# Kernel optimization log

Hardware: AMD Instinct MI355X
Metric: run time of the kernel (lower is better)

Reference implementation:

```python
import jax, jax.numpy as jnp
import numpy as np

N_NODES = 100_000
N_EDGES = 1_000_000
NODE_DIM = 64
EDGE_DIM = 32
EPS = 1e-5
SLOPE = 0.1  # LeakyReLU negative slope


def _mlp2(v, W1, b1, W2, b2):
    # Linear -> LeakyReLU(0.1) -> (dropout = identity in eval) -> Linear
    h = jax.nn.leaky_relu(v @ W1 + b1, negative_slope=SLOPE)
    return h @ W2 + b2


def setup_inputs() -> dict:
    key = jax.random.key(0)
    ks = jax.random.split(key, 8)
    s = 0.05  # small init scale for weights
    return {
        "x": jax.random.normal(ks[0], (N_NODES, NODE_DIM), dtype=jnp.float32),
        "edge_attr": jax.random.normal(ks[1], (N_EDGES, EDGE_DIM), dtype=jnp.float32),
        # node_transform: Linear(D, 2D) -> Linear(2D, D)
        "W1n": jax.random.normal(ks[2], (NODE_DIM, 2 * NODE_DIM), dtype=jnp.float32) * s,
        "b1n": jnp.zeros((2 * NODE_DIM,), dtype=jnp.float32),
        "W2n": jax.random.normal(ks[3], (2 * NODE_DIM, NODE_DIM), dtype=jnp.float32) * s,
        "b2n": jnp.zeros((NODE_DIM,), dtype=jnp.float32),
        # edge_feature_transform: Linear(ED, D) -> Linear(D, D)
        "W1e": jax.random.normal(ks[4], (EDGE_DIM, NODE_DIM), dtype=jnp.float32) * s,
        "b1e": jnp.zeros((NODE_DIM,), dtype=jnp.float32),
        "W2e": jax.random.normal(ks[5], (NODE_DIM, NODE_DIM), dtype=jnp.float32) * s,
        "b2e": jnp.zeros((NODE_DIM,), dtype=jnp.float32),
        "res_w": jnp.ones((1,), dtype=jnp.float32),
        "dp_scale": jnp.ones((1,), dtype=jnp.float32),
        "gamma": jnp.ones((NODE_DIM,), dtype=jnp.float32),
        "beta": jnp.zeros((NODE_DIM,), dtype=jnp.float32),
        "edge_index": jax.random.randint(ks[6], (2, N_EDGES), 0, N_NODES, dtype=jnp.int64)
        if jax.config.jax_enable_x64 else jax.random.randint(ks[6], (2, N_EDGES), 0, N_NODES, dtype=jnp.int32),
    }


def reference(x, edge_attr, W1n, b1n, W2n, b2n, W1e, b1e, W2e, b2e,
              res_w, dp_scale, gamma, beta, edge_index):
    num_nodes = x.shape[0]
    # node_transform MLP on all nodes
    x_t = _mlp2(x, W1n, b1n, W2n, b2n)                 # [N, D]
    # edge_feature_transform MLP on all edges
    e_t = _mlp2(edge_attr, W1e, b1e, W2e, b2e)         # [E, D]
    src, dst = edge_index[0], edge_index[1]
    # per-edge gather-mul-scale, scatter-add into dst nodes
    msgs = x_t[src] * e_t * dp_scale                   # [E, D]
    aggregated = jax.ops.segment_sum(msgs, dst, num_segments=num_nodes)  # [N, D]
    out = x + aggregated * res_w
    # LayerNorm over last dim (dropout is identity in eval)
    mu = jnp.mean(out, axis=-1, keepdims=True)
    var = jnp.mean(jnp.square(out - mu), axis=-1, keepdims=True)
    return (out - mu) * jax.lax.rsqrt(var + EPS) * gamma + beta
```

## Files before the change

### kernel.cpp

```cpp
#include <hip/hip_runtime.h>
#include <hip/hip_bf16.h>

#define N_NODES 100000
#define N_EDGES 1000000
#define EPS 1e-5f
#define SLOPE 0.1f

typedef __attribute__((ext_vector_type(8))) short short8;
typedef __attribute__((ext_vector_type(4))) float f32x4;

#define MFMA16(a, b, c) __builtin_amdgcn_mfma_f32_16x16x32_bf16(a, b, c, 0, 0, 0)

__device__ __forceinline__ float lrelu(float v) { return v > 0.f ? v : SLOPE * v; }

__device__ __forceinline__ unsigned short f2bf(float f) {
  __hip_bfloat16 h = __float2bfloat16(f);
  return __builtin_bit_cast(unsigned short, h);
}
__device__ __forceinline__ unsigned pk2(float lo, float hi) {
  return (unsigned)f2bf(lo) | ((unsigned)f2bf(hi) << 16);
}
__device__ __forceinline__ float blo(unsigned u) { return __uint_as_float(u << 16); }
__device__ __forceinline__ float bhi(unsigned u) { return __uint_as_float(u & 0xffff0000u); }

__device__ __forceinline__ short8 mk_frag8(const float v[8]) {
  uint4 u;
  u.x = pk2(v[0], v[1]);
  u.y = pk2(v[2], v[3]);
  u.z = pk2(v[4], v[5]);
  u.w = pk2(v[6], v[7]);
  return __builtin_bit_cast(short8, u);
}

#if __has_builtin(__builtin_amdgcn_global_atomic_fadd_v2bf16)
#define AGG_BF16 1
typedef __attribute__((ext_vector_type(2))) short bf16x2;
typedef __attribute__((address_space(1))) bf16x2 gbf16x2;
__device__ __forceinline__ void atomic_pk_bf16(void* p, unsigned packed) {
  __builtin_amdgcn_global_atomic_fadd_v2bf16((gbf16x2*)(unsigned long long)p,
                                             __builtin_bit_cast(bf16x2, packed));
}
#else
#define AGG_BF16 0
#endif

__global__ __launch_bounds__(256) void node_mfma(const float* __restrict__ x,
                                                 const float* __restrict__ W1n,
                                                 const float* __restrict__ b1n,
                                                 const float* __restrict__ W2n,
                                                 const float* __restrict__ b2n,
                                                 __hip_bfloat16* __restrict__ xt) {
  const int lane = threadIdx.x & 63;
  const int lo = lane & 15;
  const int G = lane >> 4;
  const int wid = (blockIdx.x * blockDim.x + threadIdx.x) >> 6;
  const int nw = (gridDim.x * blockDim.x) >> 6;

  short8 A1[8][2];
#pragma unroll
  for (int t = 0; t < 8; ++t)
#pragma unroll
    for (int kt = 0; kt < 2; ++kt) {
      float v[8];
#pragma unroll
      for (int j = 0; j < 8; ++j) v[j] = W1n[(kt * 32 + G * 8 + j) * 128 + t * 16 + lo];
      A1[t][kt] = mk_frag8(v);
    }
  short8 A2[4][4];
#pragma unroll
  for (int ct = 0; ct < 4; ++ct)
#pragma unroll
    for (int kt = 0; kt < 4; ++kt) {
      float v[8];
#pragma unroll
      for (int j = 0; j < 8; ++j) v[j] = W2n[(kt * 32 + G * 8 + j) * 64 + ct * 16 + lo];
      A2[ct][kt] = mk_frag8(v);
    }
  const f32x4 zero = {0.f, 0.f, 0.f, 0.f};

  for (int tile = wid; tile < N_NODES / 16; tile += nw) {
    const int n0 = tile * 16;
    short8 B1[2];
#pragma unroll
    for (int kt = 0; kt < 2; ++kt) {
      const float* p = &x[(size_t)(n0 + lo) * 64 + kt * 32 + G * 8];
      float4 q0 = *(const float4*)p;
      float4 q1 = *(const float4*)(p + 4);
      float v[8] = {q0.x, q0.y, q0.z, q0.w, q1.x, q1.y, q1.z, q1.w};
      B1[kt] = mk_frag8(v);
    }
    unsigned P[8][2];
#pragma unroll
    for (int t = 0; t < 8; ++t) {
      f32x4 d = MFMA16(A1[t][0], B1[0], zero);
      d = MFMA16(A1[t][1], B1[1], d);
      const float4 bv = *(const float4*)&b1n[t * 16 + G * 4];
      P[t][0] = pk2(lrelu(d[0] + bv.x), lrelu(d[1] + bv.y));
      P[t][1] = pk2(lrelu(d[2] + bv.z), lrelu(d[3] + bv.w));
    }
    f32x4 D2[4] = {zero, zero, zero, zero};
#pragma unroll
    for (int kt = 0; kt < 4; ++kt) {
      unsigned u[4];
#pragma unroll
      for (int i = 0; i < 4; ++i) {
        const int srcidx = lo + 16 * (2 * (G & 1) + (i >> 1));
        unsigned r0 = (unsigned)__shfl((int)P[kt * 2][i & 1], srcidx);
        unsigned r1 = (unsigned)__shfl((int)P[kt * 2 + 1][i & 1], srcidx);
        u[i] = (lane >= 32) ? r1 : r0;
      }
      uint4 uu;
      uu.x = u[0]; uu.y = u[1]; uu.z = u[2]; uu.w = u[3];
      short8 B2 = __builtin_bit_cast(short8, uu);
#pragma unroll
      for (int ct = 0; ct < 4; ++ct) D2[ct] = MFMA16(A2[ct][kt], B2, D2[ct]);
    }
    unsigned short* row = (unsigned short*)xt + (size_t)(n0 + lo) * 64;
#pragma unroll
    for (int ct = 0; ct < 4; ++ct) {
      const float4 bv = *(const float4*)&b2n[ct * 16 + G * 4];
      uint2 s;
      s.x = pk2(D2[ct][0] + bv.x, D2[ct][1] + bv.y);
      s.y = pk2(D2[ct][2] + bv.z, D2[ct][3] + bv.w);
      *(uint2*)(row + ct * 16 + G * 4) = s;
    }
  }
}

__global__ __launch_bounds__(256) void edge_mfma(const float* __restrict__ ea,
                                                 const int* __restrict__ ei,
                                                 const float* __restrict__ W1e,
                                                 const float* __restrict__ b1e,
                                                 const float* __restrict__ W2e,
                                                 const float* __restrict__ b2e,
                                                 const __hip_bfloat16* __restrict__ xt,
                                                 const float* __restrict__ dp,
                                                 void* __restrict__ aggv) {
  const int lane = threadIdx.x & 63;
  const int lo = lane & 15;
  const int G = lane >> 4;
  const int w = threadIdx.x >> 6;
  const int wid = (blockIdx.x * blockDim.x + threadIdx.x) >> 6;
  const int nw = (gridDim.x * blockDim.x) >> 6;
  const float scale = dp[0];

  __shared__ float msg_lds[4][16 * 68];
  float* ml = &msg_lds[w][0];

  short8 A1[4];
#pragma unroll
  for (int t = 0; t < 4; ++t) {
    float v[8];
#pragma unroll
    for (int j = 0; j < 8; ++j) v[j] = W1e[(G * 8 + j) * 64 + t * 16 + lo];
    A1[t] = mk_frag8(v);
  }
  short8 A2[4][2];
#pragma unroll
  for (int t = 0; t < 4; ++t)
#pragma unroll
    for (int kt = 0; kt < 2; ++kt) {
      float v[8];
#pragma unroll
      for (int j = 0; j < 8; ++j) v[j] = W2e[(kt * 32 + G * 8 + j) * 64 + t * 16 + lo];
      A2[t][kt] = mk_frag8(v);
    }
  f32x4 Cb1[4], Cb2[4];
#pragma unroll
  for (int t = 0; t < 4; ++t)
#pragma unroll
    for (int r = 0; r < 4; ++r) {
      Cb1[t][r] = b1e[t * 16 + G * 4 + r];
      Cb2[t][r] = b2e[t * 16 + G * 4 + r];
    }

  for (int tile = wid; tile < N_EDGES / 16; tile += nw) {
    const int e0 = tile * 16;
    const int srcv = ei[e0 + lo];
    const int dstv = ei[N_EDGES + e0 + lo];
    const float* p = &ea[(size_t)(e0 + lo) * 32 + G * 8];
    float4 q0 = *(const float4*)p;
    float4 q1 = *(const float4*)(p + 4);
    float v[8] = {q0.x, q0.y, q0.z, q0.w, q1.x, q1.y, q1.z, q1.w};
    short8 B1 = mk_frag8(v);

    unsigned P[4][2];
#pragma unroll
    for (int t = 0; t < 4; ++t) {
      f32x4 d = MFMA16(A1[t], B1, Cb1[t]);
      P[t][0] = pk2(lrelu(d[0]), lrelu(d[1]));
      P[t][1] = pk2(lrelu(d[2]), lrelu(d[3]));
    }
    short8 B2f[2];
#pragma unroll
    for (int kt = 0; kt < 2; ++kt) {
      unsigned u[4];
#pragma unroll
      for (int i = 0; i < 4; ++i) {
        const int srcidx = lo + 16 * (2 * (G & 1) + (i >> 1));
        unsigned r0 = (unsigned)__shfl((int)P[kt * 2][i & 1], srcidx);
        unsigned r1 = (unsigned)__shfl((int)P[kt * 2 + 1][i & 1], srcidx);
        u[i] = (lane >= 32) ? r1 : r0;
      }
      uint4 uu;
      uu.x = u[0]; uu.y = u[1]; uu.z = u[2]; uu.w = u[3];
      B2f[kt] = __builtin_bit_cast(short8, uu);
    }
#pragma unroll
    for (int t = 0; t < 4; ++t) {
      f32x4 d = MFMA16(A2[t][0], B2f[0], Cb2[t]);
      d = MFMA16(A2[t][1], B2f[1], d);
      f32x4 sv;
#pragma unroll
      for (int r = 0; r < 4; ++r) sv[r] = d[r] * scale;
      *(f32x4*)&ml[lo * 68 + t * 16 + G * 4] = sv;
    }

#if AGG_BF16
    const int half = lane >> 5;
    const int l2 = lane & 31;
    unsigned short* aggb = (unsigned short*)aggv;
#pragma unroll
    for (int ep = 0; ep < 8; ++ep) {
      const int e = 2 * ep + half;
      const int se = __shfl(srcv, e);
      const int de = __shfl(dstv, e);
      const float2 m = *(const float2*)&ml[e * 68 + 2 * l2];
      const unsigned g = *(const unsigned*)((const unsigned short*)xt + (size_t)se * 64 + 2 * l2);
      atomic_pk_bf16(aggb + (size_t)de * 64 + 2 * l2, pk2(blo(g) * m.x, bhi(g) * m.y));
    }
#else
    float* agg = (float*)aggv;
#pragma unroll
    for (int eb = 0; eb < 2; ++eb) {
      float msg[8];
      int des[8];
#pragma unroll
      for (int i = 0; i < 8; ++i) {
        const int e = eb * 8 + i;
        const int se = __builtin_amdgcn_readlane(srcv, e);
        des[i] = __builtin_amdgcn_readlane(dstv, e);
        const float m = ml[e * 68 + lane];
        const unsigned short xb = ((const unsigned short*)xt)[(size_t)se * 64 + lane];
        msg[i] = __uint_as_float((unsigned)xb << 16) * m;
      }
#pragma unroll
      for (int i = 0; i < 8; ++i)
        unsafeAtomicAdd(agg + (size_t)des[i] * 64 + lane, msg[i]);
    }
#endif
  }
}

__global__ __launch_bounds__(256) void finalize(const float* __restrict__ x,
                                                const void* __restrict__ aggv,
                                                const float* __restrict__ res_w,
                                                const float* __restrict__ gamma,
                                                const float* __restrict__ beta,
                                                float* __restrict__ out) {
  const int lane = threadIdx.x & 63;
  const int wid = (blockIdx.x * blockDim.x + threadIdx.x) >> 6;
  const int nw = (gridDim.x * blockDim.x) >> 6;
  const float rw = res_w[0];
  const float g = gamma[lane], bb = beta[lane];
  for (int n = wid; n < N_NODES; n += nw) {
#if AGG_BF16
    const unsigned short ab = ((const unsigned short*)aggv)[(size_t)n * 64 + lane];
    const float a = __uint_as_float((unsigned)ab << 16);
#else
    const float a = ((const float*)aggv)[(size_t)n * 64 + lane];
#endif
    float v = fmaf(a, rw, x[(size_t)n * 64 + lane]);
    float s = v;
#pragma unroll
    for (int off = 1; off < 64; off <<= 1) s += __shfl_xor(s, off);
    const float mu = s * (1.f / 64.f);
    const float d = v - mu;
    float s2 = d * d;
#pragma unroll
    for (int off = 1; off < 64; off <<= 1) s2 += __shfl_xor(s2, off);
    out[(size_t)n * 64 + lane] = fmaf(d * rsqrtf(s2 * (1.f / 64.f) + EPS), g, bb);
  }
}

extern "C" void kernel_launch(void* const* d_in, const int* in_sizes, int n_in,
                              void* d_out, int out_size, void* d_ws, size_t ws_size,
                              hipStream_t stream) {
  const float* x = (const float*)d_in[0];
  const float* edge_attr = (const float*)d_in[1];
  const float* W1n = (const float*)d_in[2];
  const float* b1n = (const float*)d_in[3];
  const float* W2n = (const float*)d_in[4];
  const float* b2n = (const float*)d_in[5];
  const float* W1e = (const float*)d_in[6];
  const float* b1e = (const float*)d_in[7];
  const float* W2e = (const float*)d_in[8];
  const float* b2e = (const float*)d_in[9];
  const float* res_w = (const float*)d_in[10];
  const float* dp_scale = (const float*)d_in[11];
  const float* gamma = (const float*)d_in[12];
  const float* beta = (const float*)d_in[13];
  const int* edge_index = (const int*)d_in[14];
  float* out = (float*)d_out;

  __hip_bfloat16* xt = (__hip_bfloat16*)d_ws;
  void* agg = (void*)((char*)d_ws + (size_t)N_NODES * 64 * sizeof(__hip_bfloat16));
#if AGG_BF16
  const size_t agg_bytes = (size_t)N_NODES * 64 * sizeof(__hip_bfloat16);
#else
  const size_t agg_bytes = (size_t)N_NODES * 64 * sizeof(float);
#endif

  hipMemsetAsync(agg, 0, agg_bytes, stream);
  node_mfma<<<1024, 256, 0, stream>>>(x, W1n, b1n, W2n, b2n, xt);
  edge_mfma<<<2048, 256, 0, stream>>>(edge_attr, edge_index, W1e, b1e, W2e, b2e,
                                      xt, dp_scale, agg);
  finalize<<<1024, 256, 0, stream>>>(x, agg, res_w, gamma, beta, out);
}
```

Before: 166.0 us.

## Fold aggregate zeroing into node kernel and prefetch edge gathers early

The separate memset of the aggregation buffer is removed, and the node kernel now zeroes it with a grid-stride loop, which saves one launch. In the edge kernel, the src/dst indices and the bf16 x_t gathers for each lane's edges are loaded at the start of each tile, so their memory latency overlaps the two MFMA layers. This replaces the later shuffles of srcv/dstv. The trade-off is higher register pressure from holding 8 indices and 8 gathered words per lane, which could lower occupancy.

```diff
diff --git a/kernel.cpp b/kernel.cpp
--- a/kernel.cpp
+++ b/kernel.cpp
@@ -49,12 +49,19 @@
                                                  const float* __restrict__ b1n,
                                                  const float* __restrict__ W2n,
                                                  const float* __restrict__ b2n,
-                                                 __hip_bfloat16* __restrict__ xt) {
+                                                 __hip_bfloat16* __restrict__ xt,
+                                                 uint4* __restrict__ agg_zero,
+                                                 int agg_zero_n) {
   const int lane = threadIdx.x & 63;
   const int lo = lane & 15;
   const int G = lane >> 4;
-  const int wid = (blockIdx.x * blockDim.x + threadIdx.x) >> 6;
-  const int nw = (gridDim.x * blockDim.x) >> 6;
+  const int tid = blockIdx.x * blockDim.x + threadIdx.x;
+  const int nt = gridDim.x * blockDim.x;
+  const int wid = tid >> 6;
+  const int nw = nt >> 6;
+
+  const uint4 z = {0u, 0u, 0u, 0u};
+  for (int i = tid; i < agg_zero_n; i += nt) agg_zero[i] = z;
 
   short8 A1[8][2];
 #pragma unroll
@@ -174,10 +181,31 @@
       Cb2[t][r] = b2e[t * 16 + G * 4 + r];
     }
 
+#if AGG_BF16
+  const int half = lane >> 5;
+  const int l2 = lane & 31;
+  unsigned short* aggb = (unsigned short*)aggv;
+#endif
+
   for (int tile = wid; tile < N_EDGES / 16; tile += nw) {
     const int e0 = tile * 16;
+
+#if AGG_BF16
+    int se_r[8], de_r[8];
+#pragma unroll
+    for (int ep = 0; ep < 8; ++ep) {
+      se_r[ep] = ei[e0 + 2 * ep + half];
+      de_r[ep] = ei[N_EDGES + e0 + 2 * ep + half];
+    }
+    unsigned g_r[8];
+#pragma unroll
+    for (int ep = 0; ep < 8; ++ep)
+      g_r[ep] = *(const unsigned*)((const unsigned short*)xt + (size_t)se_r[ep] * 64 + 2 * l2);
+#else
     const int srcv = ei[e0 + lo];
     const int dstv = ei[N_EDGES + e0 + lo];
+#endif
+
     const float* p = &ea[(size_t)(e0 + lo) * 32 + G * 8];
     float4 q0 = *(const float4*)p;
     float4 q1 = *(const float4*)(p + 4);
@@ -217,17 +245,12 @@
     }
 
 #if AGG_BF16
-    const int half = lane >> 5;
-    const int l2 = lane & 31;
-    unsigned short* aggb = (unsigned short*)aggv;
 #pragma unroll
     for (int ep = 0; ep < 8; ++ep) {
       const int e = 2 * ep + half;
-      const int se = __shfl(srcv, e);
-      const int de = __shfl(dstv, e);
       const float2 m = *(const float2*)&ml[e * 68 + 2 * l2];
-      const unsigned g = *(const unsigned*)((const unsigned short*)xt + (size_t)se * 64 + 2 * l2);
-      atomic_pk_bf16(aggb + (size_t)de * 64 + 2 * l2, pk2(blo(g) * m.x, bhi(g) * m.y));
+      const unsigned g = g_r[ep];
+      atomic_pk_bf16(aggb + (size_t)de_r[ep] * 64 + 2 * l2, pk2(blo(g) * m.x, bhi(g) * m.y));
     }
 #else
     float* agg = (float*)aggv;
@@ -311,8 +334,8 @@
   const size_t agg_bytes = (size_t)N_NODES * 64 * sizeof(float);
 #endif
 
-  hipMemsetAsync(agg, 0, agg_bytes, stream);
-  node_mfma<<<1024, 256, 0, stream>>>(x, W1n, b1n, W2n, b2n, xt);
+  node_mfma<<<1024, 256, 0, stream>>>(x, W1n, b1n, W2n, b2n, xt,
+                                      (uint4*)agg, (int)(agg_bytes / 16));
   edge_mfma<<<2048, 256, 0, stream>>>(edge_attr, edge_index, W1e, b1e, W2e, b2e,
                                       xt, dp_scale, agg);
   finalize<<<1024, 256, 0, stream>>>(x, agg, res_w, gamma, beta, out);
```

After: 155.0 us. -6.6%, faster.
